# Optimization experiments

Hardware: AMD Instinct MI355X
Metric: run time of the kernel (lower is better)

The kernel has to match this reference:

```python
import jax, jax.numpy as jnp
import numpy as np

SEQ, BATCH, HIDDEN = 2048, 2, 1024
NUM_HEADS, HEAD_DIM = 16, 64
LN_EPS = 1e-6
NEG_INF = -1e10


def setup_inputs() -> dict:
    key = jax.random.key(0)
    k1, k2, k3 = jax.random.split(key, 3)
    inputs_q = jax.random.normal(k1, (SEQ, BATCH, HIDDEN), dtype=jnp.float32)
    ln_scale = jnp.ones((HIDDEN,), dtype=jnp.float32)
    ln_bias = jnp.zeros((HIDDEN,), dtype=jnp.float32)
    # fused QKV kernel: (hidden, 3, num_heads*head_dim), fan_in variance scaling
    qkv_kernel = jax.random.normal(k2, (HIDDEN, 3, NUM_HEADS * HEAD_DIM), dtype=jnp.float32) / np.sqrt(HIDDEN).astype(np.float32)
    out_kernel = jax.random.normal(k3, (NUM_HEADS * HEAD_DIM, HIDDEN), dtype=jnp.float32) / np.sqrt(NUM_HEADS * HEAD_DIM).astype(np.float32)
    return {"inputs_q": inputs_q, "ln_scale": ln_scale, "ln_bias": ln_bias,
            "qkv_kernel": qkv_kernel, "out_kernel": out_kernel}


def reference(inputs_q, ln_scale, ln_bias, qkv_kernel, out_kernel):
    s, b, h = inputs_q.shape
    # --- LayerNorm (fused with QKV projection in the original module) ---
    mu = jnp.mean(inputs_q, axis=-1, keepdims=True)
    var = jnp.mean(jnp.square(inputs_q - mu), axis=-1, keepdims=True)
    ln_out = (inputs_q - mu) * jax.lax.rsqrt(var + LN_EPS) * ln_scale + ln_bias
    # --- fused QKV projection: (s,b,h) @ (h,3,nh*hd) -> (s,b,3,nh*hd) ---
    qkv = jnp.einsum('sbh,htk->stbk', ln_out, qkv_kernel)  # (s,3,b,nh*hd)
    q = qkv[:, 0].reshape(s, b, NUM_HEADS, HEAD_DIM)  # (s,b,nh,hd)
    k = qkv[:, 1].reshape(s, b, NUM_HEADS, HEAD_DIM)
    v = qkv[:, 2].reshape(s, b, NUM_HEADS, HEAD_DIM)
    # --- core attention (transpose_batch_sequence=True layout) ---
    scale = 1.0 / np.sqrt(HEAD_DIM).astype(np.float32)  # scale_attn_logits=True
    logits = jnp.einsum('qbhd,kbhd->bhqk', q, k) * scale
    causal = jnp.tril(jnp.ones((s, s), dtype=bool))  # attn_mask_type='causal'
    logits = jnp.where(causal[None, None], logits, jnp.asarray(NEG_INF, logits.dtype))
    attn = jax.nn.softmax(logits, axis=-1)
    ctx = jnp.einsum('bhqk,kbhd->qbhd', attn, v).reshape(s, b, NUM_HEADS * HEAD_DIM)
    # --- output projection ---
    return jnp.einsum('sbk,kh->sbh', ctx, out_kernel)
```

## Files before the change

kernel.cpp:

```cpp
#include <hip/hip_runtime.h>

typedef unsigned short u16;
typedef unsigned int u32;
typedef __attribute__((ext_vector_type(8))) short short8;
typedef __attribute__((ext_vector_type(4))) float f32x4;

#define AS1C(p) ((const __attribute__((address_space(1))) void*)(p))
#define AS3(p)  ((__attribute__((address_space(3))) void*)(p))

constexpr int SEQ = 2048, BATCH = 2, HIDDEN = 1024, NH = 16, HD = 64;
constexpr int MROWS = SEQ * BATCH;
constexpr int QKV_N = 3 * NH * HD;
#define Q_SCALE 0.18033688011112042f

__device__ __forceinline__ float bf2f(u16 u) {
  union { u32 i; float f; } v; v.i = (u32)u << 16; return v.f;
}
__device__ __forceinline__ u16 f2bf(float f) {
  union { float f; u32 i; } v; v.f = f;
  u32 r = v.i + 0x7fffu + ((v.i >> 16) & 1u);
  return (u16)(r >> 16);
}
__device__ __forceinline__ u32 cvt_pk_bf16(float lo, float hi) {
  u32 r;
  asm("v_cvt_pk_bf16_f32 %0, %1, %2" : "=v"(r) : "v"(lo), "v"(hi));
  return r;
}
__device__ __forceinline__ bool is_f32(const unsigned* probe) { return probe[0] == 0x3F800000u; }

__global__ __launch_bounds__(256) void transpose_k(const void* __restrict__ in,
                                                   u16* __restrict__ out, int R, int C,
                                                   const unsigned* __restrict__ probe) {
  __shared__ alignas(16) u16 t[32][33];
  const bool fm = is_f32(probe);
  int c0 = blockIdx.x * 32, r0 = blockIdx.y * 32;
  int tx = threadIdx.x & 31, ty = threadIdx.x >> 5;
  if (fm) {
    const float* fin = (const float*)in;
#pragma unroll
    for (int i = 0; i < 32; i += 8) t[ty + i][tx] = f2bf(fin[(size_t)(r0 + ty + i) * C + c0 + tx]);
  } else {
    const u16* uin = (const u16*)in;
#pragma unroll
    for (int i = 0; i < 32; i += 8) t[ty + i][tx] = uin[(size_t)(r0 + ty + i) * C + c0 + tx];
  }
  __syncthreads();
#pragma unroll
  for (int i = 0; i < 32; i += 8) out[(size_t)(c0 + ty + i) * R + r0 + tx] = t[tx][ty + i];
}

__global__ __launch_bounds__(256) void ln_k(const void* __restrict__ xv, const void* __restrict__ gv,
                                            const void* __restrict__ bv, u16* __restrict__ y,
                                            const unsigned* __restrict__ probe) {
  const bool fm = is_f32(probe);
  int row = blockIdx.x, t = threadIdx.x;
  float f0, f1, f2, f3, g0, g1, g2, g3, b0, b1, b2, b3;
  if (fm) {
    float4 v = *(const float4*)((const float*)xv + (size_t)row * HIDDEN + t * 4);
    f0 = v.x; f1 = v.y; f2 = v.z; f3 = v.w;
    float4 gg = *(const float4*)((const float*)gv + t * 4);
    g0 = gg.x; g1 = gg.y; g2 = gg.z; g3 = gg.w;
    float4 bb = *(const float4*)((const float*)bv + t * 4);
    b0 = bb.x; b1 = bb.y; b2 = bb.z; b3 = bb.w;
  } else {
    ushort4 v = *(const ushort4*)((const u16*)xv + (size_t)row * HIDDEN + t * 4);
    f0 = bf2f(v.x); f1 = bf2f(v.y); f2 = bf2f(v.z); f3 = bf2f(v.w);
    ushort4 gg = *(const ushort4*)((const u16*)gv + t * 4);
    g0 = bf2f(gg.x); g1 = bf2f(gg.y); g2 = bf2f(gg.z); g3 = bf2f(gg.w);
    ushort4 bb = *(const ushort4*)((const u16*)bv + t * 4);
    b0 = bf2f(bb.x); b1 = bf2f(bb.y); b2 = bf2f(bb.z); b3 = bf2f(bb.w);
  }
  float s = f0 + f1 + f2 + f3;
  float s2 = f0 * f0 + f1 * f1 + f2 * f2 + f3 * f3;
#pragma unroll
  for (int off = 1; off < 64; off <<= 1) { s += __shfl_xor(s, off); s2 += __shfl_xor(s2, off); }
  __shared__ float ps[4], ps2[4];
  int w = t >> 6, lane = t & 63;
  if (lane == 0) { ps[w] = s; ps2[w] = s2; }
  __syncthreads();
  s = ps[0] + ps[1] + ps[2] + ps[3];
  s2 = ps2[0] + ps2[1] + ps2[2] + ps2[3];
  float mu = s * (1.0f / HIDDEN);
  float rstd = rsqrtf(s2 * (1.0f / HIDDEN) - mu * mu + 1e-6f);
  ushort4 o;
  o.x = f2bf((f0 - mu) * rstd * g0 + b0);
  o.y = f2bf((f1 - mu) * rstd * g1 + b1);
  o.z = f2bf((f2 - mu) * rstd * g2 + b2);
  o.w = f2bf((f3 - mu) * rstd * g3 + b3);
  *(ushort4*)(y + (size_t)row * HIDDEN + t * 4) = o;
}

template <int EPI>
__global__ __launch_bounds__(256) void gemm_k(const u16* __restrict__ A, const u16* __restrict__ Bt,
                                              void* __restrict__ o0, u16* __restrict__ o1,
                                              u16* __restrict__ o2, int M, int N, int K,
                                              const unsigned* __restrict__ probe) {
  __shared__ alignas(16) u16 As[2][128 * 32];
  __shared__ alignas(16) u16 Bs[2][128 * 32];
  const int bm = blockIdx.x, bn = blockIdx.y;
  const int tid = threadIdx.x, w = tid >> 6, lane = tid & 63;
  const int wr = w >> 1, wc = w & 1, lr = lane & 15, lk = lane >> 4;
  f32x4 acc[4][4] = {};

  const int srow_lo = lane >> 2;
  const int sslot = lane & 3;
  const int csw = ((lk ^ ((lr >> 1) & 3)) * 8);
  const int nk = K >> 5;

  int srowA[2], srcA[2];
#pragma unroll
  for (int j = 0; j < 2; j++) {
    const int issue = w * 2 + j;
    srowA[j] = issue * 16 + srow_lo;
    srcA[j] = ((sslot ^ ((srowA[j] >> 1) & 3)) * 8);
  }

#define STAGE(kt, bufi)                                                                     \
  {                                                                                         \
    const int k0s = (kt) * 32;                                                              \
    _Pragma("unroll")                                                                       \
    for (int j = 0; j < 2; j++) {                                                           \
      const int issue = w * 2 + j;                                                          \
      __builtin_amdgcn_global_load_lds(                                                     \
          AS1C(A + (size_t)(bm * 128 + srowA[j]) * K + k0s + srcA[j]),                      \
          AS3(As[bufi] + issue * 512 + lane * 8), 16, 0, 0);                                \
      __builtin_amdgcn_global_load_lds(                                                     \
          AS1C(Bt + (size_t)(bn * 128 + srowA[j]) * K + k0s + srcA[j]),                     \
          AS3(Bs[bufi] + issue * 512 + lane * 8), 16, 0, 0);                                \
    }                                                                                       \
  }

  STAGE(0, 0);
  __syncthreads();

  int buf = 0;
  for (int kt = 0; kt < nk; ++kt) {
    if (kt + 1 < nk) STAGE(kt + 1, buf ^ 1);
    short8 a[4], b[4];
#pragma unroll
    for (int i = 0; i < 4; i++) {
      a[i] = *(const short8*)(As[buf] + (wr * 64 + i * 16 + lr) * 32 + csw);
      b[i] = *(const short8*)(Bs[buf] + (wc * 64 + i * 16 + lr) * 32 + csw);
    }
#pragma unroll
    for (int mi = 0; mi < 4; mi++)
#pragma unroll
      for (int ni = 0; ni < 4; ni++)
        acc[mi][ni] = __builtin_amdgcn_mfma_f32_16x16x32_bf16(a[mi], b[ni], acc[mi][ni], 0, 0, 0);
    __syncthreads();
    buf ^= 1;
  }
#undef STAGE

  const int r0 = bm * 128 + wr * 64, c0 = bn * 128 + wc * 64;
  if constexpr (EPI == 0) {
    const bool fm = is_f32(probe);
#pragma unroll
    for (int mi = 0; mi < 4; mi++)
#pragma unroll
      for (int ni = 0; ni < 4; ni++) {
        int col = c0 + ni * 16 + lr;
#pragma unroll
        for (int j = 0; j < 4; j++) {
          int row = r0 + mi * 16 + lk * 4 + j;
          if (fm) ((float*)o0)[(size_t)row * N + col] = acc[mi][ni][j];
          else    ((u16*)o0)[(size_t)row * N + col] = f2bf(acc[mi][ni][j]);
        }
      }
  } else {
#pragma unroll
    for (int mi = 0; mi < 4; mi++)
#pragma unroll
      for (int ni = 0; ni < 4; ni++) {
        int n = c0 + ni * 16 + lr;
        int t = n >> 10, rem = n & 1023, h = rem >> 6, d = rem & 63;
#pragma unroll
        for (int j = 0; j < 4; j++) {
          int r = r0 + mi * 16 + lk * 4 + j;
          int s = r >> 1, bb = r & 1;
          size_t bh = (size_t)(bb * NH + h);
          if (t == 0)      ((u16*)o0)[(bh * SEQ + s) * HD + d] = f2bf(acc[mi][ni][j] * Q_SCALE);
          else if (t == 1) o1[(bh * SEQ + s) * HD + d] = f2bf(acc[mi][ni][j]);
          else             o2[(bh * HD + d) * SEQ + s] = f2bf(acc[mi][ni][j]);
        }
      }
  }
}

__global__ __launch_bounds__(256, 3) void attn_k(const u16* __restrict__ Q, const u16* __restrict__ Kb,
                                                 const u16* __restrict__ VT, u16* __restrict__ ctx) {
  const int flat = blockIdx.x;
  const int xu = flat & 7, idx = flat >> 3;
  const int bh = xu * 4 + (idx & 3);
  const int qt = 31 - (idx >> 2);
  const int tid = threadIdx.x;
  const int w = tid >> 6, lane = tid & 63;
  const int lr = lane & 15, lk = lane >> 4;
  const size_t base = (size_t)bh * SEQ * HD;
  const int b = bh >> 4, h = bh & 15;

  __shared__ alignas(16) u16 Ks[2][4096];
  __shared__ alignas(16) u16 Vs[2][4096];
  __shared__ alignas(16) u16 P[4][16 * 72];
  u16* Pw = &P[w][0];
  u32* Pw32 = (u32*)Pw;

  const int st_r = lane >> 3;
  const int st_c = 8 * ((lane & 7) ^ st_r);

  const int qr0 = qt * 64 + w * 16;
  const int qrow = qr0 + lr;
  const int klast = qt;

  short8 aq[2];
#pragma unroll
  for (int kk = 0; kk < 2; kk++)
    aq[kk] = *(const short8*)(Q + base + (size_t)qrow * HD + kk * 32 + lk * 8);

  f32x4 o[4] = {};
  float m = -1e30f, l = 0.0f;

#pragma unroll
  for (int j = 0; j < 2; j++) {
    const int c = j * 4 + w;
    const int r = c * 8 + st_r;
    __builtin_amdgcn_global_load_lds(AS1C(Kb + base + (size_t)r * HD + st_c),
                                     AS3(Ks[0] + c * 512), 16, 0, 0);
    __builtin_amdgcn_global_load_lds(AS1C(VT + base + (size_t)r * SEQ + st_c),
                                     AS3(Vs[0] + c * 512), 16, 0, 0);
  }
  __syncthreads();

  for (int kt = 0; kt <= klast; kt++) {
    const int k0 = kt * 64;
    const int buf = kt & 1;
    if (kt < klast) {
      const int kn = k0 + 64;
#pragma unroll
      for (int j = 0; j < 2; j++) {
        const int c = j * 4 + w;
        const int r = c * 8 + st_r;
        __builtin_amdgcn_global_load_lds(AS1C(Kb + base + (size_t)(kn + r) * HD + st_c),
                                         AS3(Ks[buf ^ 1] + c * 512), 16, 0, 0);
        __builtin_amdgcn_global_load_lds(AS1C(VT + base + (size_t)r * SEQ + kn + st_c),
                                         AS3(Vs[buf ^ 1] + c * 512), 16, 0, 0);
      }
    }
    const int swz = (lr & 7) << 3;
    short8 bk[4][2], bv[4][2];
#pragma unroll
    for (int ni = 0; ni < 4; ni++) {
      const int row = ni * 16 + lr;
#pragma unroll
      for (int kk = 0; kk < 2; kk++)
        bk[ni][kk] = *(const short8*)(Ks[buf] + row * 64 + ((kk * 32 + lk * 8) ^ swz));
#pragma unroll
      for (int ks = 0; ks < 2; ks++)
        bv[ni][ks] = *(const short8*)(Vs[buf] + row * 64 + ((ks * 32 + lk * 8) ^ swz));
    }
    f32x4 s[4] = {};
    __builtin_amdgcn_s_setprio(1);
#pragma unroll
    for (int ni = 0; ni < 4; ni++)
#pragma unroll
      for (int kk = 0; kk < 2; kk++)
        s[ni] = __builtin_amdgcn_mfma_f32_16x16x32_bf16(bk[ni][kk], aq[kk], s[ni], 0, 0, 0);
    __builtin_amdgcn_s_setprio(0);
    if (kt == klast) {
#pragma unroll
      for (int ni = 0; ni < 4; ni++)
#pragma unroll
        for (int j = 0; j < 4; j++)
          if (k0 + ni * 16 + lk * 4 + j > qrow) s[ni][j] = -1e30f;
    }
    float pmn[4];
#pragma unroll
    for (int ni = 0; ni < 4; ni++)
      pmn[ni] = fmaxf(fmaxf(s[ni][0], s[ni][1]), fmaxf(s[ni][2], s[ni][3]));
    float pm = fmaxf(fmaxf(pmn[0], pmn[1]), fmaxf(pmn[2], pmn[3]));
    pm = fmaxf(pm, __shfl_xor(pm, 16));
    pm = fmaxf(pm, __shfl_xor(pm, 32));
    if (!__all(pm - m <= 8.0f)) {
      const float nm = fmaxf(m, pm);
      const float fac = exp2f(m - nm);
      m = nm;
      l *= fac;
      float f0 = __shfl(fac, lk * 4 + 0);
      float f1 = __shfl(fac, lk * 4 + 1);
      float f2 = __shfl(fac, lk * 4 + 2);
      float f3 = __shfl(fac, lk * 4 + 3);
#pragma unroll
      for (int ni = 0; ni < 4; ni++) {
        o[ni][0] *= f0; o[ni][1] *= f1; o[ni][2] *= f2; o[ni][3] *= f3;
      }
    }
    float rsn[4];
#pragma unroll
    for (int ni = 0; ni < 4; ni++) {
#pragma unroll
      for (int j = 0; j < 4; j++) s[ni][j] = exp2f(s[ni][j] - m);
      rsn[ni] = (s[ni][0] + s[ni][1]) + (s[ni][2] + s[ni][3]);
    }
    float rs = (rsn[0] + rsn[1]) + (rsn[2] + rsn[3]);
    rs += __shfl_xor(rs, 16);
    rs += __shfl_xor(rs, 32);
    l += rs;
#pragma unroll
    for (int ni = 0; ni < 4; ni++) {
      uint2 pk;
      pk.x = cvt_pk_bf16(s[ni][0], s[ni][1]);
      pk.y = cvt_pk_bf16(s[ni][2], s[ni][3]);
      *(uint2*)(Pw32 + lr * 36 + ni * 8 + lk * 2) = pk;
    }
    short8 pa[2];
#pragma unroll
    for (int kk = 0; kk < 2; kk++)
      pa[kk] = *(const short8*)(Pw + lr * 72 + kk * 32 + lk * 8);
    __builtin_amdgcn_s_setprio(1);
#pragma unroll
    for (int ni = 0; ni < 4; ni++)
#pragma unroll
      for (int kk = 0; kk < 2; kk++)
        o[ni] = __builtin_amdgcn_mfma_f32_16x16x32_bf16(pa[kk], bv[ni][kk], o[ni], 0, 0, 0);
    __builtin_amdgcn_s_setprio(0);
    __syncthreads();
  }
  float linv0 = 1.0f / __shfl(l, lk * 4 + 0);
  float linv1 = 1.0f / __shfl(l, lk * 4 + 1);
  float linv2 = 1.0f / __shfl(l, lk * 4 + 2);
  float linv3 = 1.0f / __shfl(l, lk * 4 + 3);
#pragma unroll
  for (int ni = 0; ni < 4; ni++) {
    int col = h * HD + ni * 16 + lr;
    ctx[(size_t)((qr0 + lk * 4 + 0) * BATCH + b) * (NH * HD) + col] = f2bf(o[ni][0] * linv0);
    ctx[(size_t)((qr0 + lk * 4 + 1) * BATCH + b) * (NH * HD) + col] = f2bf(o[ni][1] * linv1);
    ctx[(size_t)((qr0 + lk * 4 + 2) * BATCH + b) * (NH * HD) + col] = f2bf(o[ni][2] * linv2);
    ctx[(size_t)((qr0 + lk * 4 + 3) * BATCH + b) * (NH * HD) + col] = f2bf(o[ni][3] * linv3);
  }
}

extern "C" void kernel_launch(void* const* d_in, const int* in_sizes, int n_in,
                              void* d_out, int out_size, void* d_ws, size_t ws_size,
                              hipStream_t stream) {
  const void* x    = d_in[0];
  const void* g    = d_in[1];
  const void* bta  = d_in[2];
  const void* wqkv = d_in[3];
  const void* wout = d_in[4];
  const unsigned* probe = (const unsigned*)d_in[1];

  char* ws = (char*)d_ws;
  u16* ln   = (u16*)(ws);
  u16* q    = (u16*)(ws + 8388608);
  u16* k    = (u16*)(ws + 16777216);
  u16* vT   = (u16*)(ws + 25165824);
  u16* qkvT = (u16*)(ws + 33554432);
  u16* outT = (u16*)(ws + 33554432 + 6291456);
  u16* ctx  = ln;

  transpose_k<<<dim3(QKV_N / 32, HIDDEN / 32), 256, 0, stream>>>(wqkv, qkvT, HIDDEN, QKV_N, probe);
  transpose_k<<<dim3(HIDDEN / 32, HIDDEN / 32), 256, 0, stream>>>(wout, outT, HIDDEN, HIDDEN, probe);
  ln_k<<<MROWS, 256, 0, stream>>>(x, g, bta, ln, probe);
  gemm_k<1><<<dim3(MROWS / 128, QKV_N / 128), 256, 0, stream>>>(ln, qkvT, q, k, vT,
                                                                MROWS, QKV_N, HIDDEN, probe);
  attn_k<<<dim3(1024), 256, 0, stream>>>(q, k, vT, ctx);
  gemm_k<0><<<dim3(MROWS / 128, HIDDEN / 128), 256, 0, stream>>>(ctx, outT, d_out, nullptr,
                                                                 nullptr, MROWS, HIDDEN,
                                                                 HIDDEN, probe);
}
```

Before: 122.8 us.

## Triple-buffer K/V tiles and software-pipeline QK^T one tile ahead in attention

```diff
diff --git a/kernel.cpp b/kernel.cpp
--- a/kernel.cpp
+++ b/kernel.cpp
@@ -187,7 +187,7 @@
   }
 }
 
-__global__ __launch_bounds__(256, 3) void attn_k(const u16* __restrict__ Q, const u16* __restrict__ Kb,
+__global__ __launch_bounds__(256, 2) void attn_k(const u16* __restrict__ Q, const u16* __restrict__ Kb,
                                                  const u16* __restrict__ VT, u16* __restrict__ ctx) {
   const int flat = blockIdx.x;
   const int xu = flat & 7, idx = flat >> 3;
@@ -199,14 +199,15 @@
   const size_t base = (size_t)bh * SEQ * HD;
   const int b = bh >> 4, h = bh & 15;
 
-  __shared__ alignas(16) u16 Ks[2][4096];
-  __shared__ alignas(16) u16 Vs[2][4096];
+  __shared__ alignas(16) u16 Ks[3 * 4096];
+  __shared__ alignas(16) u16 Vs[3 * 4096];
   __shared__ alignas(16) u16 P[4][16 * 72];
   u16* Pw = &P[w][0];
   u32* Pw32 = (u32*)Pw;
 
   const int st_r = lane >> 3;
   const int st_c = 8 * ((lane & 7) ^ st_r);
+  const int swz = (lr & 7) << 3;
 
   const int qr0 = qt * 64 + w * 16;
   const int qrow = qr0 + lr;
@@ -220,63 +221,79 @@
   f32x4 o[4] = {};
   float m = -1e30f, l = 0.0f;
 
-#pragma unroll
-  for (int j = 0; j < 2; j++) {
-    const int c = j * 4 + w;
-    const int r = c * 8 + st_r;
-    __builtin_amdgcn_global_load_lds(AS1C(Kb + base + (size_t)r * HD + st_c),
-                                     AS3(Ks[0] + c * 512), 16, 0, 0);
-    __builtin_amdgcn_global_load_lds(AS1C(VT + base + (size_t)r * SEQ + st_c),
-                                     AS3(Vs[0] + c * 512), 16, 0, 0);
-  }
-  __syncthreads();
+#define ASTAGE(kt_, bi_)                                                                    \
+  {                                                                                         \
+    const int kn_ = (kt_) * 64;                                                             \
+    _Pragma("unroll")                                                                       \
+    for (int j = 0; j < 2; j++) {                                                           \
+      const int c = j * 4 + w;                                                              \
+      const int r = c * 8 + st_r;                                                           \
+      __builtin_amdgcn_global_load_lds(AS1C(Kb + base + (size_t)(kn_ + r) * HD + st_c),     \
+                                       AS3(Ks + (bi_) * 4096 + c * 512), 16, 0, 0);         \
+      __builtin_amdgcn_global_load_lds(AS1C(VT + base + (size_t)r * SEQ + kn_ + st_c),      \
+                                       AS3(Vs + (bi_) * 4096 + c * 512), 16, 0, 0);         \
+    }                                                                                       \
+  }
+
+  ASTAGE(0, 0);
+  if (klast >= 1) ASTAGE(1, 1);
+
+  int bc = 0, bnx = 1, bst = 2;
+  f32x4 sc[4], sn[4];
 
   for (int kt = 0; kt <= klast; kt++) {
-    const int k0 = kt * 64;
-    const int buf = kt & 1;
+    __syncthreads();
+    if (kt + 2 <= klast) ASTAGE(kt + 2, bst);
+    if (kt == 0) {
+      short8 bk[4][2];
+#pragma unroll
+      for (int ni = 0; ni < 4; ni++)
+#pragma unroll
+        for (int kk = 0; kk < 2; kk++)
+          bk[ni][kk] = *(const short8*)(Ks + bc * 4096 + (ni * 16 + lr) * 64 + ((kk * 32 + lk * 8) ^ swz));
+#pragma unroll
+      for (int ni = 0; ni < 4; ni++) {
+        sc[ni] = f32x4{0.f, 0.f, 0.f, 0.f};
+#pragma unroll
+        for (int kk = 0; kk < 2; kk++)
+          sc[ni] = __builtin_amdgcn_mfma_f32_16x16x32_bf16(bk[ni][kk], aq[kk], sc[ni], 0, 0, 0);
+      }
+    }
     if (kt < klast) {
-      const int kn = k0 + 64;
-#pragma unroll
-      for (int j = 0; j < 2; j++) {
-        const int c = j * 4 + w;
-        const int r = c * 8 + st_r;
-        __builtin_amdgcn_global_load_lds(AS1C(Kb + base + (size_t)(kn + r) * HD + st_c),
-                                         AS3(Ks[buf ^ 1] + c * 512), 16, 0, 0);
-        __builtin_amdgcn_global_load_lds(AS1C(VT + base + (size_t)r * SEQ + kn + st_c),
-                                         AS3(Vs[buf ^ 1] + c * 512), 16, 0, 0);
-      }
-    }
-    const int swz = (lr & 7) << 3;
-    short8 bk[4][2], bv[4][2];
-#pragma unroll
-    for (int ni = 0; ni < 4; ni++) {
-      const int row = ni * 16 + lr;
-#pragma unroll
-      for (int kk = 0; kk < 2; kk++)
-        bk[ni][kk] = *(const short8*)(Ks[buf] + row * 64 + ((kk * 32 + lk * 8) ^ swz));
+      short8 bk[4][2];
+#pragma unroll
+      for (int ni = 0; ni < 4; ni++)
+#pragma unroll
+        for (int kk = 0; kk < 2; kk++)
+          bk[ni][kk] = *(const short8*)(Ks + bnx * 4096 + (ni * 16 + lr) * 64 + ((kk * 32 + lk * 8) ^ swz));
+      __builtin_amdgcn_s_setprio(1);
+#pragma unroll
+      for (int ni = 0; ni < 4; ni++) {
+        sn[ni] = f32x4{0.f, 0.f, 0.f, 0.f};
+#pragma unroll
+        for (int kk = 0; kk < 2; kk++)
+          sn[ni] = __builtin_amdgcn_mfma_f32_16x16x32_bf16(bk[ni][kk], aq[kk], sn[ni], 0, 0, 0);
+      }
+      __builtin_amdgcn_s_setprio(0);
+    }
+    short8 bv[4][2];
+#pragma unroll
+    for (int ni = 0; ni < 4; ni++)
 #pragma unroll
       for (int ks = 0; ks < 2; ks++)
-        bv[ni][ks] = *(const short8*)(Vs[buf] + row * 64 + ((ks * 32 + lk * 8) ^ swz));
-    }
-    f32x4 s[4] = {};
-    __builtin_amdgcn_s_setprio(1);
+        bv[ni][ks] = *(const short8*)(Vs + bc * 4096 + (ni * 16 + lr) * 64 + ((ks * 32 + lk * 8) ^ swz));
+    if (kt == klast) {
+      const int k0 = kt * 64;
+#pragma unroll
+      for (int ni = 0; ni < 4; ni++)
+#pragma unroll
+        for (int j = 0; j < 4; j++)
+          if (k0 + ni * 16 + lk * 4 + j > qrow) sc[ni][j] = -1e30f;
+    }
+    float pmn[4];
 #pragma unroll
     for (int ni = 0; ni < 4; ni++)
-#pragma unroll
-      for (int kk = 0; kk < 2; kk++)
-        s[ni] = __builtin_amdgcn_mfma_f32_16x16x32_bf16(bk[ni][kk], aq[kk], s[ni], 0, 0, 0);
-    __builtin_amdgcn_s_setprio(0);
-    if (kt == klast) {
-#pragma unroll
-      for (int ni = 0; ni < 4; ni++)
-#pragma unroll
-        for (int j = 0; j < 4; j++)
-          if (k0 + ni * 16 + lk * 4 + j > qrow) s[ni][j] = -1e30f;
-    }
-    float pmn[4];
-#pragma unroll
-    for (int ni = 0; ni < 4; ni++)
-      pmn[ni] = fmaxf(fmaxf(s[ni][0], s[ni][1]), fmaxf(s[ni][2], s[ni][3]));
+      pmn[ni] = fmaxf(fmaxf(sc[ni][0], sc[ni][1]), fmaxf(sc[ni][2], sc[ni][3]));
     float pm = fmaxf(fmaxf(pmn[0], pmn[1]), fmaxf(pmn[2], pmn[3]));
     pm = fmaxf(pm, __shfl_xor(pm, 16));
     pm = fmaxf(pm, __shfl_xor(pm, 32));
@@ -294,22 +311,17 @@
         o[ni][0] *= f0; o[ni][1] *= f1; o[ni][2] *= f2; o[ni][3] *= f3;
       }
     }
-    float rsn[4];
 #pragma unroll
     for (int ni = 0; ni < 4; ni++) {
 #pragma unroll
-      for (int j = 0; j < 4; j++) s[ni][j] = exp2f(s[ni][j] - m);
-      rsn[ni] = (s[ni][0] + s[ni][1]) + (s[ni][2] + s[ni][3]);
-    }
-    float rs = (rsn[0] + rsn[1]) + (rsn[2] + rsn[3]);
-    rs += __shfl_xor(rs, 16);
-    rs += __shfl_xor(rs, 32);
-    l += rs;
+      for (int j = 0; j < 4; j++) sc[ni][j] = exp2f(sc[ni][j] - m);
+      l += (sc[ni][0] + sc[ni][1]) + (sc[ni][2] + sc[ni][3]);
+    }
 #pragma unroll
     for (int ni = 0; ni < 4; ni++) {
       uint2 pk;
-      pk.x = cvt_pk_bf16(s[ni][0], s[ni][1]);
-      pk.y = cvt_pk_bf16(s[ni][2], s[ni][3]);
+      pk.x = cvt_pk_bf16(sc[ni][0], sc[ni][1]);
+      pk.y = cvt_pk_bf16(sc[ni][2], sc[ni][3]);
       *(uint2*)(Pw32 + lr * 36 + ni * 8 + lk * 2) = pk;
     }
     short8 pa[2];
@@ -323,12 +335,18 @@
       for (int kk = 0; kk < 2; kk++)
         o[ni] = __builtin_amdgcn_mfma_f32_16x16x32_bf16(pa[kk], bv[ni][kk], o[ni], 0, 0, 0);
     __builtin_amdgcn_s_setprio(0);
-    __syncthreads();
-  }
-  float linv0 = 1.0f / __shfl(l, lk * 4 + 0);
-  float linv1 = 1.0f / __shfl(l, lk * 4 + 1);
-  float linv2 = 1.0f / __shfl(l, lk * 4 + 2);
-  float linv3 = 1.0f / __shfl(l, lk * 4 + 3);
+#pragma unroll
+    for (int ni = 0; ni < 4; ni++) sc[ni] = sn[ni];
+    const int t_ = bc; bc = bnx; bnx = bst; bst = t_;
+  }
+#undef ASTAGE
+  float lf = l;
+  lf += __shfl_xor(lf, 16);
+  lf += __shfl_xor(lf, 32);
+  float linv0 = 1.0f / __shfl(lf, lk * 4 + 0);
+  float linv1 = 1.0f / __shfl(lf, lk * 4 + 1);
+  float linv2 = 1.0f / __shfl(lf, lk * 4 + 2);
+  float linv3 = 1.0f / __shfl(lf, lk * 4 + 3);
 #pragma unroll
   for (int ni = 0; ni < 4; ni++) {
     int col = h * HD + ni * 16 + lr;
```

New measurement: 124.5 us. Within noise of the previous version (+1.4%).
